# Kernel optimization log

Hardware: AMD Instinct MI355X
Metric: run time of the kernel (lower is better)

The kernel has to match this reference:

```python
import jax, jax.numpy as jnp
import numpy as np

N = 8192
F_IN = 128
F_OUT = 64
NEG_INF = -9e15


def setup_inputs() -> dict:
    key = jax.random.key(0)
    k1, k2, k3, k4 = jax.random.split(key, 4)
    x = jax.random.normal(k1, (N, F_IN), dtype=jnp.float32)
    adj = jax.random.randint(k2, (N, N), 0, 2, dtype=jnp.int32)
    W = jax.random.normal(k3, (F_OUT, F_IN), dtype=jnp.float32) * 0.05  # torch Linear weight [out,in]
    a = jax.random.normal(k4, (1, 2 * F_OUT), dtype=jnp.float32) * 0.05  # attention vector weight [1, 2*out]
    return {"x": x, "adj": adj, "W": W, "a": a}


def reference(x, adj, W, a):
    fout = W.shape[0]
    Wh = x @ W.T                                   # [N, out]
    a1 = a[0, :fout]                               # a.weight.T[:out]
    a2 = a[0, fout:]                               # a.weight.T[out:]
    Wh1 = Wh @ a1                                  # [N]
    Wh2 = Wh @ a2                                  # [N]
    e = jax.nn.leaky_relu(Wh1[:, None] + Wh2[None, :], negative_slope=0.2)  # [N, N]
    attention = jnp.where(adj > 0, e, NEG_INF)
    attention = jax.nn.softmax(attention, axis=1)
    # dropout is identity in eval / deterministic reference
    h_prime = attention @ Wh                       # [N, out]
    return jax.nn.elu(h_prime)
```

## Files before the change

### kernel.cpp

```cpp
#include <hip/hip_runtime.h>
#include <cstdint>
#include <cstddef>

#define NN 8192
#define FIN 128
#define FOUT 64

typedef __attribute__((ext_vector_type(8))) short short8;
typedef __attribute__((ext_vector_type(4))) float f32x4;

__device__ __forceinline__ unsigned short f32_to_bf16_bits(float f) {
    union { float f; uint32_t u; } c; c.f = f;
    uint32_t u = c.u;
    u += 0x7fffu + ((u >> 16) & 1u);
    return (unsigned short)(u >> 16);
}

__device__ __forceinline__ unsigned int pack_bf16(float lo, float hi) {
    return (unsigned int)f32_to_bf16_bits(lo) |
           ((unsigned int)f32_to_bf16_bits(hi) << 16);
}

__global__ __launch_bounds__(256) void gat_prep(
    const float* __restrict__ x, const float* __restrict__ W,
    const float* __restrict__ a, unsigned short* __restrict__ WhT,
    float* __restrict__ Wh1, float* __restrict__ Wh2)
{
    const int t    = threadIdx.x;
    const int f    = t & 63;
    const int iloc = t >> 6;
    const int i    = blockIdx.x * 4 + iloc;

    const float4* x4 = (const float4*)(x + (size_t)i * FIN);
    const float4* w4 = (const float4*)(W + (size_t)f * FIN);

    float acc = 0.f;
#pragma unroll
    for (int k = 0; k < FIN / 4; ++k) {
        float4 xv = x4[k];
        float4 wv = w4[k];
        acc += xv.x * wv.x + xv.y * wv.y + xv.z * wv.z + xv.w * wv.w;
    }

    WhT[(size_t)f * NN + i] = f32_to_bf16_bits(acc);

    float r1 = acc * a[f];
    float r2 = acc * a[64 + f];
#pragma unroll
    for (int m = 1; m < 64; m <<= 1) {
        r1 += __shfl_xor(r1, m, 64);
        r2 += __shfl_xor(r2, m, 64);
    }
    if (f == 0) { Wh1[i] = r1; Wh2[i] = r2; }
}

__global__ __launch_bounds__(256, 4) void gat_attn(
    const int* __restrict__ adj, const unsigned short* __restrict__ WhT,
    const float* __restrict__ Wh1, const float* __restrict__ Wh2,
    float* __restrict__ Cpart, float* __restrict__ Tpart)
{
    __shared__ float lds_C[4][16][68];
    __shared__ float lds_tot[4][16];

    const int tid  = threadIdx.x;
    const int wave = tid >> 6;
    const int lane = tid & 63;
    const int il   = lane & 15;
    const int q    = lane >> 4;
    const int rt   = blockIdx.x >> 1;
    const int jh   = blockIdx.x & 1;
    const int i0   = rt * 16;
    const int i    = i0 + il;

    const float wh1   = Wh1[i];
    const int   jbase = jh * 4096 + wave * 32 + q * 8;
    const int* __restrict__ adjrow = adj + (size_t)i * NN;

    const short8* bp0 = (const short8*)(WhT + (size_t)(0  + il) * NN);
    const short8* bp1 = (const short8*)(WhT + (size_t)(16 + il) * NN);
    const short8* bp2 = (const short8*)(WhT + (size_t)(32 + il) * NN);
    const short8* bp3 = (const short8*)(WhT + (size_t)(48 + il) * NN);

    f32x4 acc0 = {0.f, 0.f, 0.f, 0.f};
    f32x4 acc1 = {0.f, 0.f, 0.f, 0.f};
    f32x4 acc2 = {0.f, 0.f, 0.f, 0.f};
    f32x4 acc3 = {0.f, 0.f, 0.f, 0.f};
    float tot = 0.f;

    int4   av0 = *(const int4*)(adjrow + jbase);
    int4   av1 = *(const int4*)(adjrow + jbase + 4);
    float4 w20 = *(const float4*)(Wh2 + jbase);
    float4 w21 = *(const float4*)(Wh2 + jbase + 4);
    int jb = jbase >> 3;
    short8 b0 = bp0[jb];
    short8 b1 = bp1[jb];
    short8 b2 = bp2[jb];
    short8 b3 = bp3[jb];

    for (int tt = 0; tt < 32; ++tt) {
        const int jn = jbase + (((tt + 1) & 31) << 7);
        const int4   nav0 = *(const int4*)(adjrow + jn);
        const int4   nav1 = *(const int4*)(adjrow + jn + 4);
        const float4 nw20 = *(const float4*)(Wh2 + jn);
        const float4 nw21 = *(const float4*)(Wh2 + jn + 4);
        const int jnb = jn >> 3;
        const short8 nb0 = bp0[jnb];
        const short8 nb1 = bp1[jnb];
        const short8 nb2 = bp2[jnb];
        const short8 nb3 = bp3[jnb];

        float wv[8];
#define CALC(idx, adjv, wh2v)                                          \
        {                                                              \
            float s = wh1 + (wh2v);                                    \
            float e = fmaxf(s, 0.2f * s);          \
            float v = ((adjv) > 0) ? __expf(e) : 0.f;                  \
            tot += v;                                                  \
            wv[idx] = v;                                               \
        }
        CALC(0, av0.x, w20.x) CALC(1, av0.y, w20.y)
        CALC(2, av0.z, w20.z) CALC(3, av0.w, w20.w)
        CALC(4, av1.x, w21.x) CALC(5, av1.y, w21.y)
        CALC(6, av1.z, w21.z) CALC(7, av1.w, w21.w)
#undef CALC

        union { short8 v; unsigned int u[4]; } af;
        af.u[0] = pack_bf16(wv[0], wv[1]);
        af.u[1] = pack_bf16(wv[2], wv[3]);
        af.u[2] = pack_bf16(wv[4], wv[5]);
        af.u[3] = pack_bf16(wv[6], wv[7]);

        acc0 = __builtin_amdgcn_mfma_f32_16x16x32_bf16(af.v, b0, acc0, 0, 0, 0);
        acc1 = __builtin_amdgcn_mfma_f32_16x16x32_bf16(af.v, b1, acc1, 0, 0, 0);
        acc2 = __builtin_amdgcn_mfma_f32_16x16x32_bf16(af.v, b2, acc2, 0, 0, 0);
        acc3 = __builtin_amdgcn_mfma_f32_16x16x32_bf16(af.v, b3, acc3, 0, 0, 0);

        av0 = nav0; av1 = nav1; w20 = nw20; w21 = nw21;
        b0 = nb0; b1 = nb1; b2 = nb2; b3 = nb3;
    }

    tot += __shfl_xor(tot, 16, 64);
    tot += __shfl_xor(tot, 32, 64);
    if (lane < 16) lds_tot[wave][lane] = tot;

#pragma unroll
    for (int r = 0; r < 4; ++r) {
        lds_C[wave][q * 4 + r][0 * 16 + il] = acc0[r];
        lds_C[wave][q * 4 + r][1 * 16 + il] = acc1[r];
        lds_C[wave][q * 4 + r][2 * 16 + il] = acc2[r];
        lds_C[wave][q * 4 + r][3 * 16 + il] = acc3[r];
    }
    __syncthreads();

#pragma unroll
    for (int e = 0; e < 4; ++e) {
        const int idx = e * 256 + tid;
        const int ii = idx >> 6;
        const int ff = idx & 63;
        float s = lds_C[0][ii][ff] + lds_C[1][ii][ff] +
                  lds_C[2][ii][ff] + lds_C[3][ii][ff];
        Cpart[((size_t)jh * NN + i0 + ii) * FOUT + ff] = s;
        if (ff == 0) {
            float ts = lds_tot[0][ii] + lds_tot[1][ii] +
                       lds_tot[2][ii] + lds_tot[3][ii];
            Tpart[(size_t)jh * NN + i0 + ii] = ts;
        }
    }
}

__global__ __launch_bounds__(256) void gat_combine(
    const float* __restrict__ Cpart, const float* __restrict__ Tpart,
    float* __restrict__ out)
{
    const int idx = blockIdx.x * 256 + threadIdx.x;
    const int i = idx >> 6;
    const float c = Cpart[idx] + Cpart[(size_t)NN * FOUT + idx];
    const float t = Tpart[i] + Tpart[NN + i];
    const float p = c / t;
    out[idx] = (p > 0.f) ? p : (__expf(p) - 1.f);
}

extern "C" void kernel_launch(void* const* d_in, const int* in_sizes, int n_in,
                              void* d_out, int out_size, void* d_ws, size_t ws_size,
                              hipStream_t stream) {
    const float* x   = (const float*)d_in[0];
    const int*   adj = (const int*)d_in[1];
    const float* W   = (const float*)d_in[2];
    const float* a   = (const float*)d_in[3];
    float* out = (float*)d_out;

    char* ws = (char*)d_ws;
    unsigned short* WhT = (unsigned short*)ws;
    float* Wh1   = (float*)(ws + (size_t)1048576);
    float* Wh2   = (float*)(ws + (size_t)1048576 + 32768);
    float* Cpart = (float*)(ws + (size_t)2097152);
    float* Tpart = (float*)(ws + (size_t)6291456);

    gat_prep<<<dim3(NN / 4), dim3(256), 0, stream>>>(x, W, a, WhT, Wh1, Wh2);
    gat_attn<<<dim3(NN / 16 * 2), dim3(256), 0, stream>>>(adj, WhT, Wh1, Wh2, Cpart, Tpart);
    gat_combine<<<dim3(NN * FOUT / 256), dim3(256), 0, stream>>>(Cpart, Tpart, out);
}
```

Baseline: 423.4 us.

## Pack adjacency into bitmask in a pre-pass and read bits in attention

Adds a kernel that reads the int32 adjacency matrix with coalesced loads and compresses it into a 1-bit-per-edge mask. The attention kernel then reads one 32-bit mask word per step instead of strided 32-byte int4 loads from 16 different rows. This is meant to remove the poorly coalesced, bandwidth-heavy adjacency traffic from the compute kernel. In exchange it adds an extra launch and a full pass over adj, needs an 8 MB workspace region, and drops the explicit register prefetch of the next iteration's loads.

```diff
diff --git a/kernel.cpp b/kernel.cpp
--- a/kernel.cpp
+++ b/kernel.cpp
@@ -21,6 +21,23 @@
            ((unsigned int)f32_to_bf16_bits(hi) << 16);
 }
 
+__global__ __launch_bounds__(256) void gat_mask(
+    const int* __restrict__ adj, unsigned int* __restrict__ maskW)
+{
+    const size_t t = (size_t)blockIdx.x * 256 + threadIdx.x;
+    const int4* p = (const int4*)(adj + t * 32);
+    unsigned int m = 0;
+#pragma unroll
+    for (int k = 0; k < 8; ++k) {
+        int4 v = p[k];
+        m |= (v.x > 0 ? 1u : 0u) << (k * 4 + 0);
+        m |= (v.y > 0 ? 1u : 0u) << (k * 4 + 1);
+        m |= (v.z > 0 ? 1u : 0u) << (k * 4 + 2);
+        m |= (v.w > 0 ? 1u : 0u) << (k * 4 + 3);
+    }
+    maskW[t] = m;
+}
+
 __global__ __launch_bounds__(256) void gat_prep(
     const float* __restrict__ x, const float* __restrict__ W,
     const float* __restrict__ a, unsigned short* __restrict__ WhT,
@@ -55,7 +72,7 @@
 }
 
 __global__ __launch_bounds__(256, 4) void gat_attn(
-    const int* __restrict__ adj, const unsigned short* __restrict__ WhT,
+    const unsigned int* __restrict__ maskW, const unsigned short* __restrict__ WhT,
     const float* __restrict__ Wh1, const float* __restrict__ Wh2,
     float* __restrict__ Cpart, float* __restrict__ Tpart)
 {
@@ -74,7 +91,8 @@
 
     const float wh1   = Wh1[i];
     const int   jbase = jh * 4096 + wave * 32 + q * 8;
-    const int* __restrict__ adjrow = adj + (size_t)i * NN;
+    const unsigned int* __restrict__ maskrow = maskW + (size_t)i * (NN / 32);
+    const int wbase = jh * 128 + wave;
 
     const short8* bp0 = (const short8*)(WhT + (size_t)(0  + il) * NN);
     const short8* bp1 = (const short8*)(WhT + (size_t)(16 + il) * NN);
@@ -87,41 +105,26 @@
     f32x4 acc3 = {0.f, 0.f, 0.f, 0.f};
     float tot = 0.f;
 
-    int4   av0 = *(const int4*)(adjrow + jbase);
-    int4   av1 = *(const int4*)(adjrow + jbase + 4);
-    float4 w20 = *(const float4*)(Wh2 + jbase);
-    float4 w21 = *(const float4*)(Wh2 + jbase + 4);
-    int jb = jbase >> 3;
-    short8 b0 = bp0[jb];
-    short8 b1 = bp1[jb];
-    short8 b2 = bp2[jb];
-    short8 b3 = bp3[jb];
-
     for (int tt = 0; tt < 32; ++tt) {
-        const int jn = jbase + (((tt + 1) & 31) << 7);
-        const int4   nav0 = *(const int4*)(adjrow + jn);
-        const int4   nav1 = *(const int4*)(adjrow + jn + 4);
-        const float4 nw20 = *(const float4*)(Wh2 + jn);
-        const float4 nw21 = *(const float4*)(Wh2 + jn + 4);
-        const int jnb = jn >> 3;
-        const short8 nb0 = bp0[jnb];
-        const short8 nb1 = bp1[jnb];
-        const short8 nb2 = bp2[jnb];
-        const short8 nb3 = bp3[jnb];
+        const int j = jbase + tt * 128;
+
+        const unsigned int mw = maskrow[wbase + tt * 4];
+        const unsigned int mb = mw >> (q * 8);
+
+        const float4 w20 = *(const float4*)(Wh2 + j);
+        const float4 w21 = *(const float4*)(Wh2 + j + 4);
 
         float wv[8];
-#define CALC(idx, adjv, wh2v)                                          \
+#define CALC(idx, wh2v)                                                \
         {                                                              \
             float s = wh1 + (wh2v);                                    \
             float e = fmaxf(s, 0.2f * s);          \
-            float v = ((adjv) > 0) ? __expf(e) : 0.f;                  \
+            float v = ((mb >> idx) & 1u) ? __expf(e) : 0.f;            \
             tot += v;                                                  \
             wv[idx] = v;                                               \
         }
-        CALC(0, av0.x, w20.x) CALC(1, av0.y, w20.y)
-        CALC(2, av0.z, w20.z) CALC(3, av0.w, w20.w)
-        CALC(4, av1.x, w21.x) CALC(5, av1.y, w21.y)
-        CALC(6, av1.z, w21.z) CALC(7, av1.w, w21.w)
+        CALC(0, w20.x) CALC(1, w20.y) CALC(2, w20.z) CALC(3, w20.w)
+        CALC(4, w21.x) CALC(5, w21.y) CALC(6, w21.z) CALC(7, w21.w)
 #undef CALC
 
         union { short8 v; unsigned int u[4]; } af;
@@ -130,13 +133,16 @@
         af.u[2] = pack_bf16(wv[4], wv[5]);
         af.u[3] = pack_bf16(wv[6], wv[7]);
 
+        const int jb = j >> 3;
+        const short8 b0 = bp0[jb];
+        const short8 b1 = bp1[jb];
+        const short8 b2 = bp2[jb];
+        const short8 b3 = bp3[jb];
+
         acc0 = __builtin_amdgcn_mfma_f32_16x16x32_bf16(af.v, b0, acc0, 0, 0, 0);
         acc1 = __builtin_amdgcn_mfma_f32_16x16x32_bf16(af.v, b1, acc1, 0, 0, 0);
         acc2 = __builtin_amdgcn_mfma_f32_16x16x32_bf16(af.v, b2, acc2, 0, 0, 0);
         acc3 = __builtin_amdgcn_mfma_f32_16x16x32_bf16(af.v, b3, acc3, 0, 0, 0);
-
-        av0 = nav0; av1 = nav1; w20 = nw20; w21 = nw21;
-        b0 = nb0; b1 = nb1; b2 = nb2; b3 = nb3;
     }
 
     tot += __shfl_xor(tot, 16, 64);
@@ -195,8 +201,10 @@
     float* Wh2   = (float*)(ws + (size_t)1048576 + 32768);
     float* Cpart = (float*)(ws + (size_t)2097152);
     float* Tpart = (float*)(ws + (size_t)6291456);
-
+    unsigned int* maskW = (unsigned int*)(ws + (size_t)8388608);
+
+    gat_mask<<<dim3((NN / 32) * NN / 256), dim3(256), 0, stream>>>(adj, maskW);
     gat_prep<<<dim3(NN / 4), dim3(256), 0, stream>>>(x, W, a, WhT, Wh1, Wh2);
-    gat_attn<<<dim3(NN / 16 * 2), dim3(256), 0, stream>>>(adj, WhT, Wh1, Wh2, Cpart, Tpart);
+    gat_attn<<<dim3(NN / 16 * 2), dim3(256), 0, stream>>>(maskW, WhT, Wh1, Wh2, Cpart, Tpart);
     gat_combine<<<dim3(NN * FOUT / 256), dim3(256), 0, stream>>>(Cpart, Tpart, out);
 }
```

New measurement: 484.7 us. 14.5% more time.
